# Performance work log

Measured on AMD Instinct MI355X. Metric: run time of the kernel, lower is better.

The kernel has to match this reference:

```python
import jax, jax.numpy as jnp
import numpy as np

D = 256                      # covariance dim, hardcoded by bottleneck Conv2d(_, 256, 1)
ITER_N = 5                   # SqrtmLayer(output, 5)
_r, _c = np.triu_indices(D)
FLAT_IDX = jnp.asarray(_r * D + _c)   # upper-tri (incl. diag) indices into flattened d*d


def setup_inputs() -> dict:
    key = jax.random.key(0)
    ks = jax.random.split(key, 5)
    B, C, H, W = 64, 2048, 16, 16
    num_classes = 4
    feats = D * (D + 1) // 2  # 32896
    return {
        "features": jax.random.normal(ks[0], (B, C, H, W), jnp.float32),
        "w_bn": jax.random.normal(ks[1], (D, C), jnp.float32) * 0.02,
        "b_bn": jnp.zeros((D,), jnp.float32),
        "w_type": jax.random.normal(ks[2], (num_classes, feats), jnp.float32) * 0.01,
        "b_type": jnp.zeros((num_classes,), jnp.float32),
        "w_flag": jax.random.normal(ks[3], (1, feats), jnp.float32) * 0.01,
        "b_flag": jnp.zeros((1,), jnp.float32),
    }


def _covpool(x):
    # x: [B, d, h, w] -> second-order pooling: x_f @ I_hat @ x_f^T, equivalent
    # to (1/M) * centered @ centered^T  (I_hat = -1/M^2 * ones + 1/M * eye)
    B, d, h, w = x.shape
    M = h * w
    xf = x.reshape(B, d, M)
    centered = xf - xf.mean(axis=2, keepdims=True)
    return jnp.einsum('bim,bjm->bij', centered, centered) / M  # [B, d, d]


def _sqrtm_ns(A, iter_n=ITER_N):
    # Newton-Schulz iteration for matrix square root (iSQRT-COV style)
    B, d, _ = A.shape
    I3 = 3.0 * jnp.eye(d, dtype=A.dtype)
    normA = jnp.trace(A, axis1=1, axis2=2)          # [B], pre-normalization
    An = A / normA[:, None, None]
    ZY = 0.5 * (I3 - An)
    Y = jnp.matmul(An, ZY)
    Z = ZY
    for _ in range(iter_n - 2):
        ZY = 0.5 * (I3 - jnp.matmul(Z, Y))
        Y = jnp.matmul(Y, ZY)
        Z = jnp.matmul(ZY, Z)
    YZY = 0.5 * jnp.matmul(Y, I3 - jnp.matmul(Z, Y))
    return YZY * jnp.sqrt(normA)[:, None, None]     # post-compensation


def reference(features, w_bn, b_bn, w_type, b_type, w_flag, b_flag):
    # 1x1 bottleneck conv: [B, C, H, W] -> [B, 256, H, W]
    x = jnp.einsum('bchw,oc->bohw', features, w_bn) + b_bn[None, :, None, None]
    cov = _covpool(x)                # [B, 256, 256]
    s = _sqrtm_ns(cov)               # [B, 256, 256]
    B = s.shape[0]
    vec = s.reshape(B, D * D)[:, FLAT_IDX]   # triu-vec: [B, 32896]
    type_logits = vec @ w_type.T + b_type    # [B, num_classes]
    flag_logits = vec @ w_flag.T + b_flag    # [B, 1]
    return (type_logits, flag_logits)
```

## Files before the change

kernel.cpp:

```cpp
#include <hip/hip_runtime.h>
#include <math.h>


typedef __attribute__((ext_vector_type(8))) short bf16x8;
typedef __attribute__((ext_vector_type(4))) float f32x4;
typedef __attribute__((ext_vector_type(4))) unsigned u32x4;
typedef __attribute__((ext_vector_type(2))) unsigned u32x2;

__device__ __forceinline__ unsigned fbits(float f) { union { float f; unsigned u; } x; x.f = f; return x.u; }
__device__ __forceinline__ float bitsf(unsigned u) { union { float f; unsigned u; } x; x.u = u; return x.f; }
__device__ __forceinline__ float bf16v(short h) { return bitsf(((unsigned)(unsigned short)h) << 16); }

__device__ __forceinline__ unsigned pack_h(float a, float b) {
  return (fbits(a) >> 16) | (fbits(b) & 0xFFFF0000u);
}
__device__ __forceinline__ unsigned pack_l(float a, float b) {
  float la = a - bitsf(fbits(a) & 0xFFFF0000u);
  float lb = b - bitsf(fbits(b) & 0xFFFF0000u);
  return (fbits(la) >> 16) | (fbits(lb) & 0xFFFF0000u);
}

__device__ __forceinline__ const bf16x8* fragp(const char* M, int kt, int row,
                                               int g, int pl) {
  return (const bf16x8*)(M + (size_t)kt * 32768 + (size_t)row * 128 +
                         ((((pl << 2) + g) ^ (row & 7)) << 4));
}
__device__ __forceinline__ const bf16x8* fragl(const char* L, int kt, int row,
                                               int g, int pl) {
  return (const bf16x8*)(L + kt * 8192 + row * 128 +
                         ((((pl << 2) + g) ^ (row & 7)) << 4));
}

__device__ __forceinline__ void write_quad_g(char* M, int row, int k0,
                                             const float* v) {
  char* rp = M + (size_t)(k0 >> 5) * 32768 + (size_t)row * 128;
  const int s = (k0 & 31) >> 3, bo = (k0 & 7) * 2;
  *(u32x2*)(rp + (((s) ^ (row & 7)) << 4) + bo) =
      (u32x2){pack_h(v[0], v[1]), pack_h(v[2], v[3])};
  *(u32x2*)(rp + (((s + 4) ^ (row & 7)) << 4) + bo) =
      (u32x2){pack_l(v[0], v[1]), pack_l(v[2], v[3])};
}
__device__ __forceinline__ void write_quad_l(char* L, int row, int k0,
                                             const float* v) {
  char* rp = L + (k0 >> 5) * 8192 + row * 128;
  const int s = (k0 & 31) >> 3, bo = (k0 & 7) * 2;
  *(u32x2*)(rp + (((s) ^ (row & 7)) << 4) + bo) =
      (u32x2){pack_h(v[0], v[1]), pack_h(v[2], v[3])};
  *(u32x2*)(rp + (((s + 4) ^ (row & 7)) << 4) + bo) =
      (u32x2){pack_l(v[0], v[1]), pack_l(v[2], v[3])};
}
__device__ __forceinline__ void read_quad_g(const char* M, int row, int k0,
                                            float* v) {
  const char* rp = M + (size_t)(k0 >> 5) * 32768 + (size_t)row * 128;
  const int s = (k0 & 31) >> 3, bo = (k0 & 7) * 2;
  const u32x2 hq = *(const u32x2*)(rp + (((s) ^ (row & 7)) << 4) + bo);
  const u32x2 lq = *(const u32x2*)(rp + (((s + 4) ^ (row & 7)) << 4) + bo);
  v[0] = bitsf(hq[0] << 16) + bitsf(lq[0] << 16);
  v[1] = bitsf(hq[0] & 0xFFFF0000u) + bitsf(lq[0] & 0xFFFF0000u);
  v[2] = bitsf(hq[1] << 16) + bitsf(lq[1] << 16);
  v[3] = bitsf(hq[1] & 0xFFFF0000u) + bitsf(lq[1] & 0xFFFF0000u);
}

#define MFMA3(c, aH, aL, bH, bL)                                            \
  c = __builtin_amdgcn_mfma_f32_16x16x32_bf16(aL, bH, c, 0, 0, 0);          \
  c = __builtin_amdgcn_mfma_f32_16x16x32_bf16(aH, bL, c, 0, 0, 0);          \
  c = __builtin_amdgcn_mfma_f32_16x16x32_bf16(aH, bH, c, 0, 0, 0);

#define LGKM_BAR() do { asm volatile("s_waitcnt lgkmcnt(0)" ::: "memory"); \
                        __builtin_amdgcn_s_barrier(); } while (0)

__global__ __launch_bounds__(256) void prep_k(
    const float* __restrict__ w_bn, const float* __restrict__ w_type,
    const float* __restrict__ w_flag, char* __restrict__ Wf,
    float* __restrict__ W2)
{
  const int bid = blockIdx.x;
  if (bid < 64) {
    const int kt = bid, r = threadIdx.x;
    const float* src = w_bn + (size_t)r * 2048 + kt * 32;
    char* rp = Wf + (size_t)kt * 32768 + (size_t)r * 128;
#pragma unroll
    for (int s = 0; s < 4; ++s) {
      float x[8];
#pragma unroll
      for (int e = 0; e < 8; ++e) x[e] = src[s * 8 + e];
      *(u32x4*)(rp + ((s ^ (r & 7)) << 4)) =
          (u32x4){pack_h(x[0], x[1]), pack_h(x[2], x[3]),
                  pack_h(x[4], x[5]), pack_h(x[6], x[7])};
      *(u32x4*)(rp + (((s + 4) ^ (r & 7)) << 4)) =
          (u32x4){pack_l(x[0], x[1]), pack_l(x[2], x[3]),
                  pack_l(x[4], x[5]), pack_l(x[6], x[7])};
    }
  } else {
    const int idx = bid - 64;
    const int v = idx >> 6, chunk = idx & 63;
    const float* src = (v < 4) ? (w_type + (size_t)v * 32896) : w_flag;
    const int e0 = chunk * 1024 + threadIdx.x * 4;
#pragma unroll
    for (int q = 0; q < 4; ++q) {
      const int e = e0 + q;
      const int i = e >> 8, j = e & 255;
      const int r = i < j ? i : j, c = i < j ? j : i;
      const int t = r * 256 - (r * (r - 1)) / 2 + (c - r);
      W2[(size_t)v * 65536 + e] = src[t] * (i == j ? 1.0f : 0.5f);
    }
  }
}

__global__ __launch_bounds__(512) void conv5_k(
    const char* __restrict__ Wf, const float* __restrict__ F,
    float* __restrict__ Xpart)
{
  __shared__ float bf32[2][64 * 33];
  __shared__ __align__(16) char bfmt[2][8192];

  const int tid = threadIdx.x, lane = tid & 63, w = tid >> 6;
  const int wr = w >> 1, wc = w & 1, fr = lane & 15, g = lane >> 4;
  const int jb = blockIdx.x * 64, bz = blockIdx.y, ks = blockIdx.z;
  const int kb = ks * 32;
  const float* Fb = F + (size_t)bz * 524288;

  const int blc = tid >> 4, blpx = (tid & 15) * 4;
  const int pkpx = tid >> 3, pkq = tid & 3, pkpl = (tid >> 2) & 1;

  f32x4 acc[4][2] = {};
  bf16x8 pa0[4][2], pa1[4][2];
  float4 bl0, bl1;

  auto bload = [&](int t, float4& r) {
    r = *(const float4*)(Fb + ((size_t)(kb + t) * 32 + blc) * 256 + jb + blpx);
  };
  auto bf32w = [&](int buf, const float4& r) {
    float* p = &bf32[buf][0];
    p[(blpx + 0) * 33 + blc] = r.x;
    p[(blpx + 1) * 33 + blc] = r.y;
    p[(blpx + 2) * 33 + blc] = r.z;
    p[(blpx + 3) * 33 + blc] = r.w;
  };
  auto aload = [&](int t, bf16x8 (*pa)[2]) {
#pragma unroll
    for (int m = 0; m < 4; ++m) {
      const int r = wr * 64 + m * 16 + fr;
#pragma unroll
      for (int pl = 0; pl < 2; ++pl) pa[m][pl] = *fragp(Wf, kb + t, r, g, pl);
    }
  };
  auto pack = [&](int buf) {
    const float* p = &bf32[buf][pkpx * 33 + pkq * 8];
    float x[8];
#pragma unroll
    for (int e = 0; e < 8; ++e) x[e] = p[e];
    u32x4 outv;
    if (pkpl == 0)
      outv = (u32x4){pack_h(x[0], x[1]), pack_h(x[2], x[3]),
                     pack_h(x[4], x[5]), pack_h(x[6], x[7])};
    else
      outv = (u32x4){pack_l(x[0], x[1]), pack_l(x[2], x[3]),
                     pack_l(x[4], x[5]), pack_l(x[6], x[7])};
    const int slot = ((pkpl << 2) + pkq) ^ (pkpx & 7);
    *(u32x4*)(&bfmt[buf][pkpx * 128 + slot * 16]) = outv;
  };
  auto gemmstep = [&](int buf, bf16x8 (*pa)[2]) {
    bf16x8 bH[2], bL[2];
#pragma unroll
    for (int n = 0; n < 2; ++n) {
      const int r = wc * 32 + n * 16 + fr;
      const char* rp = &bfmt[buf][r * 128];
      bH[n] = *(const bf16x8*)(rp + ((g ^ (r & 7)) << 4));
      bL[n] = *(const bf16x8*)(rp + (((g + 4) ^ (r & 7)) << 4));
    }
#pragma unroll
    for (int m = 0; m < 4; ++m)
#pragma unroll
      for (int n = 0; n < 2; ++n) {
        f32x4 c = acc[m][n];
        MFMA3(c, pa[m][0], pa[m][1], bH[n], bL[n]);
        acc[m][n] = c;
      }
  };

  bload(0, bl0);
  bf32w(0, bl0);
  bload(1, bl1);
  aload(0, pa0);
  LGKM_BAR();
  bf32w(1, bl1);
  pack(0);
  aload(1, pa1);
  bload(2, bl0);
  LGKM_BAR();

  for (int t2 = 0; t2 < 32; t2 += 2) {
    gemmstep(0, pa0);
    if (t2 + 1 < 32) pack(1);
    if (t2 + 2 < 32) { bf32w(0, bl0); aload(t2 + 2, pa0); }
    if (t2 + 3 < 32) bload(t2 + 3, bl1);
    LGKM_BAR();
    gemmstep(1, pa1);
    if (t2 + 2 < 32) pack(0);
    if (t2 + 3 < 32) { bf32w(1, bl1); aload(t2 + 3, pa1); }
    if (t2 + 4 < 32) bload(t2 + 4, bl0);
    LGKM_BAR();
  }

  float* Xp = Xpart + ((size_t)ks * 64 + bz) * 65536;
#pragma unroll
  for (int m = 0; m < 4; ++m) {
    const int gi0 = wr * 64 + m * 16 + g * 4;
#pragma unroll
    for (int n = 0; n < 2; ++n) {
      const int gj = jb + wc * 32 + n * 16 + fr;
#pragma unroll
      for (int j = 0; j < 4; ++j)
        Xp[(size_t)(gi0 + j) * 256 + gj] = acc[m][n][j];
    }
  }
}

__global__ __launch_bounds__(256) void combine_k(
    const float* __restrict__ Xp0, const float* __restrict__ Xp1,
    const float* __restrict__ bias, char* __restrict__ X,
    float* __restrict__ mu, float* __restrict__ nrm_part)
{
  const int chunk = blockIdx.x, bz = blockIdx.y;
  const int tid = threadIdx.x, lane = tid & 63, w = tid >> 6;
  const float* p0 = Xp0 + (size_t)bz * 65536;
  const float* p1 = Xp1 + (size_t)bz * 65536;
  char* Xb = X + (size_t)bz * 262144;
  float tracc = 0.f;
#pragma unroll
  for (int i = 0; i < 8; ++i) {
    const int r = chunk * 32 + w * 8 + i;
    const float4 a = *(const float4*)(p0 + (size_t)r * 256 + lane * 4);
    const float4 b = *(const float4*)(p1 + (size_t)r * 256 + lane * 4);
    const float bi = bias[r];
    float v[4] = {a.x + b.x + bi, a.y + b.y + bi,
                  a.z + b.z + bi, a.w + b.w + bi};
    float s = v[0] + v[1] + v[2] + v[3];
    float ss = v[0] * v[0] + v[1] * v[1] + v[2] * v[2] + v[3] * v[3];
#pragma unroll
    for (int o = 32; o > 0; o >>= 1) {
      s += __shfl_down(s, o);
      ss += __shfl_down(ss, o);
    }
    const float st = __shfl(s, 0), sst = __shfl(ss, 0);
    const float m = st * (1.f / 256.f);
    if (lane == 0) mu[bz * 256 + r] = m;
    tracc += sst * (1.f / 256.f) - m * m;
    write_quad_g(Xb, r, lane * 4, v);
  }
  __shared__ float red[4];
  if (lane == 0) red[w] = tracc;
  __syncthreads();
  if (tid == 0)
    nrm_part[bz * 8 + chunk] = red[0] + red[1] + red[2] + red[3];
}

__device__ __forceinline__ float nrm_sum(const float* nrmp, int bz) {
  float nv = 0.f;
#pragma unroll
  for (int q = 0; q < 8; ++q) nv += nrmp[bz * 8 + q];
  return nv;
}

template <int MODE>
__global__ __launch_bounds__(512) void col_k(
    const char* __restrict__ A1, const char* __restrict__ Bsrc,
    const char* __restrict__ Ys, const char* __restrict__ Zs,
    char* __restrict__ outA, char* __restrict__ outB,
    const float* __restrict__ mu, const float* __restrict__ nrmp,
    float* __restrict__ Sf)
{
  __shared__ __align__(16) char Plds[65536];
  const int tid = threadIdx.x, lane = tid & 63, w = tid >> 6;
  const int fr = lane & 15, g = lane >> 4;
  const int blk = blockIdx.x;
  const int bz = (blk & 7) * 8 + ((blk >> 3) & 7);
  const int jb = (blk >> 6) * 64;
  const size_t MB = 262144;
  const char* Ab = A1 + (size_t)bz * MB;
  const char* Bb = Bsrc + (size_t)bz * MB;
  const int r0 = g * 4;

  f32x4 acc[2][4] = {};
  {
    bf16x8 pa[2][2][2], pb[2][4][2];
#pragma unroll
    for (int par = 0; par < 2; ++par) {
#pragma unroll
      for (int m = 0; m < 2; ++m) {
        const int r = w * 32 + m * 16 + fr;
#pragma unroll
        for (int pl = 0; pl < 2; ++pl) pa[par][m][pl] = *fragp(Ab, par, r, g, pl);
      }
#pragma unroll
      for (int n = 0; n < 4; ++n) {
        const int r = jb + n * 16 + fr;
#pragma unroll
        for (int pl = 0; pl < 2; ++pl) pb[par][n][pl] = *fragp(Bb, par, r, g, pl);
      }
    }
    for (int t2 = 0; t2 < 8; t2 += 2) {
#pragma unroll
      for (int par = 0; par < 2; ++par) {
        const int t = t2 + par;
        bf16x8 aH[2], aL[2], bH[4], bL[4];
#pragma unroll
        for (int m = 0; m < 2; ++m) { aH[m] = pa[par][m][0]; aL[m] = pa[par][m][1]; }
#pragma unroll
        for (int n = 0; n < 4; ++n) { bH[n] = pb[par][n][0]; bL[n] = pb[par][n][1]; }
        if (t + 2 < 8) {
#pragma unroll
          for (int m = 0; m < 2; ++m) {
            const int r = w * 32 + m * 16 + fr;
#pragma unroll
            for (int pl = 0; pl < 2; ++pl)
              pa[par][m][pl] = *fragp(Ab, t + 2, r, g, pl);
          }
#pragma unroll
          for (int n = 0; n < 4; ++n) {
            const int r = jb + n * 16 + fr;
#pragma unroll
            for (int pl = 0; pl < 2; ++pl)
              pb[par][n][pl] = *fragp(Bb, t + 2, r, g, pl);
          }
        }
#pragma unroll
        for (int m = 0; m < 2; ++m)
#pragma unroll
          for (int n = 0; n < 4; ++n) {
            f32x4 c = acc[m][n];
            MFMA3(c, aH[m], aL[m], bH[n], bL[n]);
            acc[m][n] = c;
          }
      }
    }
  }

  if constexpr (MODE == 0) {
    const float rn = 1.0f / nrm_sum(nrmp, bz);
    const float* mub = mu + bz * 256;
    char* oA = outA + (size_t)bz * MB;
    char* oB = outB + (size_t)bz * MB;
#pragma unroll
    for (int m = 0; m < 2; ++m) {
      const int gi0 = w * 32 + m * 16 + r0;
#pragma unroll
      for (int n = 0; n < 4; ++n) {
        const int gj = jb + n * 16 + fr;
        float vv[4], zz[4];
#pragma unroll
        for (int j = 0; j < 4; ++j) {
          const float v =
              (acc[m][n][j] * (1.f / 256.f) - mub[gi0 + j] * mub[gj]) * rn;
          vv[j] = v;
          zz[j] = (gi0 + j == gj ? 1.5f : 0.f) - 0.5f * v;
        }
        write_quad_g(oA, gj, gi0, vv);
        write_quad_g(oB, gj, gi0, zz);
      }
    }
  } else if constexpr (MODE == 1) {
    char* oA = outA + (size_t)bz * MB;
#pragma unroll
    for (int m = 0; m < 2; ++m) {
      const int gi0 = w * 32 + m * 16 + r0;
#pragma unroll
      for (int n = 0; n < 4; ++n) {
        const int gj = jb + n * 16 + fr;
        float av[4], vv[4];
        read_quad_g(Bb, gj, gi0, av);
#pragma unroll
        for (int j = 0; j < 4; ++j) vv[j] = 1.5f * av[j] - 0.5f * acc[m][n][j];
        write_quad_g(oA, gj, gi0, vv);
      }
    }
  } else {
#pragma unroll
    for (int m = 0; m < 2; ++m) {
      const int gi0 = w * 32 + m * 16 + r0;
#pragma unroll
      for (int n = 0; n < 4; ++n) {
        const int jl = n * 16 + fr;
        float vv[4] = {acc[m][n][0], acc[m][n][1], acc[m][n][2], acc[m][n][3]};
        write_quad_l(Plds, jl, gi0, vv);
      }
    }
    const char* Yb = Ys + (size_t)bz * MB;
    const char* Zb = (MODE == 2) ? (Zs + (size_t)bz * MB) : nullptr;
    bf16x8 py[2][2][2], pz[2][2][2];
#pragma unroll
    for (int par = 0; par < 2; ++par)
#pragma unroll
      for (int m = 0; m < 2; ++m) {
        const int r = w * 32 + m * 16 + fr;
#pragma unroll
        for (int pl = 0; pl < 2; ++pl) {
          py[par][m][pl] = *fragp(Yb, par, r, g, pl);
          if constexpr (MODE == 2) pz[par][m][pl] = *fragp(Zb, par, r, g, pl);
        }
      }
    __syncthreads();

    f32x4 aY[2][4] = {}, aZ[2][4] = {};
    for (int t2 = 0; t2 < 8; t2 += 2) {
#pragma unroll
      for (int par = 0; par < 2; ++par) {
        const int t = t2 + par;
        bf16x8 yH[2], yL[2], zH[2], zL[2];
#pragma unroll
        for (int m = 0; m < 2; ++m) {
          yH[m] = py[par][m][0]; yL[m] = py[par][m][1];
          if constexpr (MODE == 2) { zH[m] = pz[par][m][0]; zL[m] = pz[par][m][1]; }
        }
        if (t + 2 < 8) {
#pragma unroll
          for (int m = 0; m < 2; ++m) {
            const int r = w * 32 + m * 16 + fr;
#pragma unroll
            for (int pl = 0; pl < 2; ++pl) {
              py[par][m][pl] = *fragp(Yb, t + 2, r, g, pl);
              if constexpr (MODE == 2) pz[par][m][pl] = *fragp(Zb, t + 2, r, g, pl);
            }
          }
        }
        bf16x8 bH[4], bL[4];
#pragma unroll
        for (int n = 0; n < 4; ++n) {
          const int jl = n * 16 + fr;
          bH[n] = *fragl(Plds, t, jl, g, 0);
          bL[n] = *fragl(Plds, t, jl, g, 1);
        }
#pragma unroll
        for (int m = 0; m < 2; ++m)
#pragma unroll
          for (int n = 0; n < 4; ++n) {
            f32x4 cy = aY[m][n];
            MFMA3(cy, yH[m], yL[m], bH[n], bL[n]);
            aY[m][n] = cy;
            if constexpr (MODE == 2) {
              f32x4 cz = aZ[m][n];
              MFMA3(cz, zH[m], zL[m], bH[n], bL[n]);
              aZ[m][n] = cz;
            }
          }
      }
    }
    if constexpr (MODE == 2) {
      char* oA = outA + (size_t)bz * MB;
      char* oB = outB + (size_t)bz * MB;
#pragma unroll
      for (int m = 0; m < 2; ++m) {
        const int gi0 = w * 32 + m * 16 + r0;
#pragma unroll
        for (int n = 0; n < 4; ++n) {
          const int gj = jb + n * 16 + fr;
          float base[4], vv[4];
          read_quad_g(Yb, gj, gi0, base);
#pragma unroll
          for (int j = 0; j < 4; ++j) vv[j] = 1.5f * base[j] - 0.5f * aY[m][n][j];
          write_quad_g(oA, gj, gi0, vv);
          read_quad_g(Zb, gj, gi0, base);
#pragma unroll
          for (int j = 0; j < 4; ++j) vv[j] = 1.5f * base[j] - 0.5f * aZ[m][n][j];
          write_quad_g(oB, gj, gi0, vv);
        }
      }
    } else {
      const float sq = sqrtf(nrm_sum(nrmp, bz));
      float* Sb = Sf + (size_t)bz * 65536;
#pragma unroll
      for (int m = 0; m < 2; ++m) {
        const int gi0 = w * 32 + m * 16 + r0;
#pragma unroll
        for (int n = 0; n < 4; ++n) {
          const int gj = jb + n * 16 + fr;
          float base[4];
          read_quad_g(Yb, gj, gi0, base);
          f32x4 vv;
#pragma unroll
          for (int j = 0; j < 4; ++j)
            vv[j] = (1.5f * base[j] - 0.5f * aY[m][n][j]) * sq;
          *(f32x4*)(Sb + (size_t)gj * 256 + gi0) = vv;
        }
      }
    }
  }
}

__global__ __launch_bounds__(256) void head2(
    const float* __restrict__ Sf, const float* __restrict__ W2,
    const float* __restrict__ b_type, const float* __restrict__ b_flag,
    float* __restrict__ out)
{
  const int b = blockIdx.x, v = blockIdx.y, tid = threadIdx.x;
  const float4* s4 = (const float4*)(Sf + (size_t)b * 65536);
  const float4* w4 = (const float4*)(W2 + (size_t)v * 65536);
  float acc = 0.f;
  for (int i = tid; i < 16384; i += 256) {
    const float4 a = s4[i], c = w4[i];
    acc += a.x * c.x + a.y * c.y + a.z * c.z + a.w * c.w;
  }
  __shared__ float red[256];
  red[tid] = acc;
  __syncthreads();
  for (int o = 128; o > 0; o >>= 1) {
    if (tid < o) red[tid] += red[tid + o];
    __syncthreads();
  }
  if (tid == 0) {
    if (v < 4) out[b * 4 + v] = red[0] + b_type[v];
    else       out[256 + b] = red[0] + b_flag[0];
  }
}

extern "C" void kernel_launch(void* const* d_in, const int* in_sizes, int n_in,
                              void* d_out, int out_size, void* d_ws, size_t ws_size,
                              hipStream_t stream)
{
  const float* features = (const float*)d_in[0];
  const float* w_bn     = (const float*)d_in[1];
  const float* b_bn     = (const float*)d_in[2];
  const float* w_type   = (const float*)d_in[3];
  const float* b_type   = (const float*)d_in[4];
  const float* w_flag   = (const float*)d_in[5];
  const float* b_flag   = (const float*)d_in[6];
  float* out = (float*)d_out;

  char* W = (char*)d_ws;
  const size_t PB = 16777216;
  char* P0 = W;           char* P1 = W + PB;     char* P2 = W + 2 * PB;
  char* P3 = W + 3 * PB;  char* P4 = W + 4 * PB;
  char* Wf = W + 5 * PB;
  float* W2 = (float*)(W + 5 * PB + 2097152);
  float* mu = (float*)(W + 5 * PB + 4194304);
  float* nrm_part = mu + 16384;
  float* Xpart = (float*)(W + 5 * PB + 8388608);
  float* Sf = (float*)P4;

  prep_k<<<dim3(384), dim3(256), 0, stream>>>(w_bn, w_type, w_flag, Wf, W2);
  conv5_k<<<dim3(4, 64, 2), dim3(512), 0, stream>>>(Wf, features, Xpart);
  combine_k<<<dim3(8, 64), dim3(256), 0, stream>>>(
      Xpart, Xpart + 64ull * 65536, b_bn, P0, mu, nrm_part);

  const dim3 cg(256), cb(512);
  col_k<0><<<cg, cb, 0, stream>>>(P0, P0, nullptr, nullptr, P1, P2, mu, nrm_part, nullptr);
  col_k<1><<<cg, cb, 0, stream>>>(P1, P1, nullptr, nullptr, P3, nullptr, nullptr, nullptr, nullptr);
  col_k<2><<<cg, cb, 0, stream>>>(P2, P3, P3, P2, P0, P4, nullptr, nullptr, nullptr);
  col_k<2><<<cg, cb, 0, stream>>>(P4, P0, P0, P4, P1, P2, nullptr, nullptr, nullptr);
  col_k<2><<<cg, cb, 0, stream>>>(P2, P1, P1, P2, P3, P0, nullptr, nullptr, nullptr);
  col_k<3><<<cg, cb, 0, stream>>>(P0, P3, P3, nullptr, nullptr, nullptr, nullptr, nrm_part, Sf);

  head2<<<dim3(64, 5), dim3(256), 0, stream>>>(Sf, W2, b_type, b_flag, out);
  (void)in_sizes; (void)n_in; (void)out_size; (void)ws_size;
}
```

Measured before the change: 287.1 us.

## Deepen conv GEMM pipeline to two k-tiles per stage with more global prefetch

```diff
diff --git a/kernel.cpp b/kernel.cpp
--- a/kernel.cpp
+++ b/kernel.cpp
@@ -107,12 +107,12 @@
   }
 }
 
-__global__ __launch_bounds__(512) void conv5_k(
+__global__ __launch_bounds__(512) void conv6_k(
     const char* __restrict__ Wf, const float* __restrict__ F,
     float* __restrict__ Xpart)
 {
-  __shared__ float bf32[2][64 * 33];
-  __shared__ __align__(16) char bfmt[2][8192];
+  __shared__ float bf32s[2][64 * 33];
+  __shared__ __align__(16) char bfmt[2][2][8192];
 
   const int tid = threadIdx.x, lane = tid & 63, w = tid >> 6;
   const int wr = w >> 1, wc = w & 1, fr = lane & 15, g = lane >> 4;
@@ -124,14 +124,13 @@
   const int pkpx = tid >> 3, pkq = tid & 3, pkpl = (tid >> 2) & 1;
 
   f32x4 acc[4][2] = {};
-  bf16x8 pa0[4][2], pa1[4][2];
-  float4 bl0, bl1;
-
-  auto bload = [&](int t, float4& r) {
-    r = *(const float4*)(Fb + ((size_t)(kb + t) * 32 + blc) * 256 + jb + blpx);
+  bf16x8 paA[4][2], paB[4][2];
+
+  auto bload = [&](int t) -> float4 {
+    return *(const float4*)(Fb + ((size_t)(kb + t) * 32 + blc) * 256 + jb + blpx);
   };
-  auto bf32w = [&](int buf, const float4& r) {
-    float* p = &bf32[buf][0];
+  auto bf32w = [&](int kk, const float4& r) {
+    float* p = &bf32s[kk][0];
     p[(blpx + 0) * 33 + blc] = r.x;
     p[(blpx + 1) * 33 + blc] = r.y;
     p[(blpx + 2) * 33 + blc] = r.z;
@@ -145,8 +144,8 @@
       for (int pl = 0; pl < 2; ++pl) pa[m][pl] = *fragp(Wf, kb + t, r, g, pl);
     }
   };
-  auto pack = [&](int buf) {
-    const float* p = &bf32[buf][pkpx * 33 + pkq * 8];
+  auto pack = [&](int kk, int dq) {
+    const float* p = &bf32s[kk][pkpx * 33 + pkq * 8];
     float x[8];
 #pragma unroll
     for (int e = 0; e < 8; ++e) x[e] = p[e];
@@ -158,14 +157,14 @@
       outv = (u32x4){pack_l(x[0], x[1]), pack_l(x[2], x[3]),
                      pack_l(x[4], x[5]), pack_l(x[6], x[7])};
     const int slot = ((pkpl << 2) + pkq) ^ (pkpx & 7);
-    *(u32x4*)(&bfmt[buf][pkpx * 128 + slot * 16]) = outv;
+    *(u32x4*)(&bfmt[dq][kk][pkpx * 128 + slot * 16]) = outv;
   };
-  auto gemmstep = [&](int buf, bf16x8 (*pa)[2]) {
+  auto gemmstep = [&](int sq, int kk, bf16x8 (*pa)[2]) {
     bf16x8 bH[2], bL[2];
 #pragma unroll
     for (int n = 0; n < 2; ++n) {
       const int r = wc * 32 + n * 16 + fr;
-      const char* rp = &bfmt[buf][r * 128];
+      const char* rp = &bfmt[sq][kk][r * 128];
       bH[n] = *(const bf16x8*)(rp + ((g ^ (r & 7)) << 4));
       bL[n] = *(const bf16x8*)(rp + (((g + 4) ^ (r & 7)) << 4));
     }
@@ -179,27 +178,37 @@
       }
   };
 
-  bload(0, bl0);
-  bf32w(0, bl0);
-  bload(1, bl1);
-  aload(0, pa0);
+  float4 b0 = bload(0), b1 = bload(1), b2 = bload(2), b3 = bload(3);
+  float4 blE0 = bload(4), blE1 = bload(5);
+  float4 blO0 = bload(6), blO1 = bload(7);
+  aload(0, paA);
+  aload(1, paB);
+
+  bf32w(0, b0); bf32w(1, b1);
   LGKM_BAR();
-  bf32w(1, bl1);
-  pack(0);
-  aload(1, pa1);
-  bload(2, bl0);
+  pack(0, 0); pack(1, 0);
   LGKM_BAR();
-
-  for (int t2 = 0; t2 < 32; t2 += 2) {
-    gemmstep(0, pa0);
-    if (t2 + 1 < 32) pack(1);
-    if (t2 + 2 < 32) { bf32w(0, bl0); aload(t2 + 2, pa0); }
-    if (t2 + 3 < 32) bload(t2 + 3, bl1);
+  bf32w(0, b2); bf32w(1, b3);
+  LGKM_BAR();
+
+  for (int pp = 0; pp < 8; ++pp) {
+    const int k4 = 4 * pp;
+    gemmstep(0, 0, paA);
+    gemmstep(0, 1, paB);
+    aload(k4 + 2, paA);
+    aload(k4 + 3, paB);
+    pack(0, 1); pack(1, 1);
     LGKM_BAR();
-    gemmstep(1, pa1);
-    if (t2 + 2 < 32) pack(0);
-    if (t2 + 3 < 32) { bf32w(1, bl1); aload(t2 + 3, pa1); }
-    if (t2 + 4 < 32) bload(t2 + 4, bl0);
+    if (pp < 7) { bf32w(0, blE0); bf32w(1, blE1); }
+    if (pp < 6) { blE0 = bload(k4 + 8); blE1 = bload(k4 + 9); }
+    LGKM_BAR();
+    gemmstep(1, 0, paA);
+    gemmstep(1, 1, paB);
+    if (pp < 7) { aload(k4 + 4, paA); aload(k4 + 5, paB); }
+    if (pp < 7) { pack(0, 0); pack(1, 0); }
+    LGKM_BAR();
+    if (pp < 7) { bf32w(0, blO0); bf32w(1, blO1); }
+    if (pp < 6) { blO0 = bload(k4 + 10); blO1 = bload(k4 + 11); }
     LGKM_BAR();
   }
 
@@ -539,7 +548,7 @@
   float* Sf = (float*)P4;
 
   prep_k<<<dim3(384), dim3(256), 0, stream>>>(w_bn, w_type, w_flag, Wf, W2);
-  conv5_k<<<dim3(4, 64, 2), dim3(512), 0, stream>>>(Wf, features, Xpart);
+  conv6_k<<<dim3(4, 64, 2), dim3(512), 0, stream>>>(Wf, features, Xpart);
   combine_k<<<dim3(8, 64), dim3(256), 0, stream>>>(
       Xpart, Xpart + 64ull * 65536, b_bn, P0, mu, nrm_part);
 
```

After: 274.4 us. -4.4%, faster.

## Load conv B-fragments directly from global and store S in head-friendly order

Applied to the files above, without the earlier changes.

```diff
diff --git a/kernel.cpp b/kernel.cpp
--- a/kernel.cpp
+++ b/kernel.cpp
@@ -9,7 +9,6 @@
 
 __device__ __forceinline__ unsigned fbits(float f) { union { float f; unsigned u; } x; x.f = f; return x.u; }
 __device__ __forceinline__ float bitsf(unsigned u) { union { float f; unsigned u; } x; x.u = u; return x.f; }
-__device__ __forceinline__ float bf16v(short h) { return bitsf(((unsigned)(unsigned short)h) << 16); }
 
 __device__ __forceinline__ unsigned pack_h(float a, float b) {
   return (fbits(a) >> 16) | (fbits(b) & 0xFFFF0000u);
@@ -66,9 +65,6 @@
   c = __builtin_amdgcn_mfma_f32_16x16x32_bf16(aH, bL, c, 0, 0, 0);          \
   c = __builtin_amdgcn_mfma_f32_16x16x32_bf16(aH, bH, c, 0, 0, 0);
 
-#define LGKM_BAR() do { asm volatile("s_waitcnt lgkmcnt(0)" ::: "memory"); \
-                        __builtin_amdgcn_s_barrier(); } while (0)
-
 __global__ __launch_bounds__(256) void prep_k(
     const float* __restrict__ w_bn, const float* __restrict__ w_type,
     const float* __restrict__ w_flag, char* __restrict__ Wf,
@@ -93,82 +89,74 @@
     }
   } else {
     const int idx = bid - 64;
-    const int v = idx >> 6, chunk = idx & 63;
+    const int v = idx >> 4, chunk = idx & 15;
     const float* src = (v < 4) ? (w_type + (size_t)v * 32896) : w_flag;
-    const int e0 = chunk * 1024 + threadIdx.x * 4;
-#pragma unroll
-    for (int q = 0; q < 4; ++q) {
-      const int e = e0 + q;
-      const int i = e >> 8, j = e & 255;
-      const int r = i < j ? i : j, c = i < j ? j : i;
-      const int t = r * 256 - (r * (r - 1)) / 2 + (c - r);
-      W2[(size_t)v * 65536 + e] = src[t] * (i == j ? 1.0f : 0.5f);
-    }
-  }
-}
-
-__global__ __launch_bounds__(512) void conv5_k(
+    const int s0 = chunk * 4096 + threadIdx.x * 16;
+    float outv[16];
+#pragma unroll
+    for (int q = 0; q < 16; ++q) {
+      const int s = s0 + q;
+      const int jbp = s >> 14, r = s & 16383;
+      const int ttid = r >> 5, qq = r & 31;
+      const int m = qq >> 4, n = (qq >> 2) & 3, jj = qq & 3;
+      const int ww = ttid >> 6, ll = ttid & 63;
+      const int i = ww * 32 + m * 16 + (ll >> 4) * 4 + jj;
+      const int jcol = jbp * 64 + n * 16 + (ll & 15);
+      const int rr = i < jcol ? i : jcol, cc = i < jcol ? jcol : i;
+      const int t = rr * 256 - (rr * (rr - 1)) / 2 + (cc - rr);
+      outv[q] = src[t] * (i == jcol ? 1.0f : 0.5f);
+    }
+    float* dst = W2 + (size_t)v * 65536 + s0;
+#pragma unroll
+    for (int q = 0; q < 4; ++q)
+      *(f32x4*)(dst + q * 4) = *(f32x4*)(outv + q * 4);
+  }
+}
+
+__global__ __launch_bounds__(512) void conv7_k(
     const char* __restrict__ Wf, const float* __restrict__ F,
     float* __restrict__ Xpart)
 {
-  __shared__ float bf32[2][64 * 33];
-  __shared__ __align__(16) char bfmt[2][8192];
-
   const int tid = threadIdx.x, lane = tid & 63, w = tid >> 6;
   const int wr = w >> 1, wc = w & 1, fr = lane & 15, g = lane >> 4;
   const int jb = blockIdx.x * 64, bz = blockIdx.y, ks = blockIdx.z;
   const int kb = ks * 32;
-  const float* Fb = F + (size_t)bz * 524288;
-
-  const int blc = tid >> 4, blpx = (tid & 15) * 4;
-  const int pkpx = tid >> 3, pkq = tid & 3, pkpl = (tid >> 2) & 1;
+  const float* Fb = F + (size_t)bz * 524288 + jb + wc * 32 + fr;
 
   f32x4 acc[4][2] = {};
-  bf16x8 pa0[4][2], pa1[4][2];
-  float4 bl0, bl1;
-
-  auto bload = [&](int t, float4& r) {
-    r = *(const float4*)(Fb + ((size_t)(kb + t) * 32 + blc) * 256 + jb + blpx);
+  bf16x8 pa[4][2];
+  float bA[16], bB[16];
+
+  auto bload = [&](int t, float* d) {
+    const float* s = Fb + ((size_t)(kb + t) * 32 + g * 8) * 256;
+#pragma unroll
+    for (int n = 0; n < 2; ++n)
+#pragma unroll
+      for (int e = 0; e < 8; ++e) d[n * 8 + e] = s[(size_t)e * 256 + n * 16];
   };
-  auto bf32w = [&](int buf, const float4& r) {
-    float* p = &bf32[buf][0];
-    p[(blpx + 0) * 33 + blc] = r.x;
-    p[(blpx + 1) * 33 + blc] = r.y;
-    p[(blpx + 2) * 33 + blc] = r.z;
-    p[(blpx + 3) * 33 + blc] = r.w;
+  auto aload = [&](int t) {
+#pragma unroll
+    for (int m = 0; m < 4; ++m)
+#pragma unroll
+      for (int pl = 0; pl < 2; ++pl)
+        pa[m][pl] = *fragp(Wf, kb + t, wr * 64 + m * 16 + fr, g, pl);
   };
-  auto aload = [&](int t, bf16x8 (*pa)[2]) {
-#pragma unroll
-    for (int m = 0; m < 4; ++m) {
-      const int r = wr * 64 + m * 16 + fr;
-#pragma unroll
-      for (int pl = 0; pl < 2; ++pl) pa[m][pl] = *fragp(Wf, kb + t, r, g, pl);
+  auto packfrag = [&](const float* x, bf16x8* bH, bf16x8* bL) {
+#pragma unroll
+    for (int n = 0; n < 2; ++n) {
+      short hh[8], ll[8];
+#pragma unroll
+      for (int e = 0; e < 8; ++e) {
+        const float v = x[n * 8 + e];
+        const unsigned u = fbits(v);
+        hh[e] = (short)(u >> 16);
+        ll[e] = (short)(fbits(v - bitsf(u & 0xFFFF0000u)) >> 16);
+      }
+      bH[n] = *(bf16x8*)hh;
+      bL[n] = *(bf16x8*)ll;
     }
   };
-  auto pack = [&](int buf) {
-    const float* p = &bf32[buf][pkpx * 33 + pkq * 8];
-    float x[8];
-#pragma unroll
-    for (int e = 0; e < 8; ++e) x[e] = p[e];
-    u32x4 outv;
-    if (pkpl == 0)
-      outv = (u32x4){pack_h(x[0], x[1]), pack_h(x[2], x[3]),
-                     pack_h(x[4], x[5]), pack_h(x[6], x[7])};
-    else
-      outv = (u32x4){pack_l(x[0], x[1]), pack_l(x[2], x[3]),
-                     pack_l(x[4], x[5]), pack_l(x[6], x[7])};
-    const int slot = ((pkpl << 2) + pkq) ^ (pkpx & 7);
-    *(u32x4*)(&bfmt[buf][pkpx * 128 + slot * 16]) = outv;
-  };
-  auto gemmstep = [&](int buf, bf16x8 (*pa)[2]) {
-    bf16x8 bH[2], bL[2];
-#pragma unroll
-    for (int n = 0; n < 2; ++n) {
-      const int r = wc * 32 + n * 16 + fr;
-      const char* rp = &bfmt[buf][r * 128];
-      bH[n] = *(const bf16x8*)(rp + ((g ^ (r & 7)) << 4));
-      bL[n] = *(const bf16x8*)(rp + (((g + 4) ^ (r & 7)) << 4));
-    }
+  auto gemm24 = [&](const bf16x8* bH, const bf16x8* bL) {
 #pragma unroll
     for (int m = 0; m < 4; ++m)
 #pragma unroll
@@ -179,28 +167,19 @@
       }
   };
 
-  bload(0, bl0);
-  bf32w(0, bl0);
-  bload(1, bl1);
-  aload(0, pa0);
-  LGKM_BAR();
-  bf32w(1, bl1);
-  pack(0);
-  aload(1, pa1);
-  bload(2, bl0);
-  LGKM_BAR();
-
+  bload(0, bA);
+  bload(1, bB);
+  aload(0);
   for (int t2 = 0; t2 < 32; t2 += 2) {
-    gemmstep(0, pa0);
-    if (t2 + 1 < 32) pack(1);
-    if (t2 + 2 < 32) { bf32w(0, bl0); aload(t2 + 2, pa0); }
-    if (t2 + 3 < 32) bload(t2 + 3, bl1);
-    LGKM_BAR();
-    gemmstep(1, pa1);
-    if (t2 + 2 < 32) pack(0);
-    if (t2 + 3 < 32) { bf32w(1, bl1); aload(t2 + 3, pa1); }
-    if (t2 + 4 < 32) bload(t2 + 4, bl0);
-    LGKM_BAR();
+    bf16x8 bH[2], bL[2];
+    packfrag(bA, bH, bL);
+    gemm24(bH, bL);
+    aload(t2 + 1);
+    if (t2 + 2 < 32) bload(t2 + 2, bA);
+    packfrag(bB, bH, bL);
+    gemm24(bH, bL);
+    if (t2 + 2 < 32) aload(t2 + 2);
+    if (t2 + 3 < 32) bload(t2 + 3, bB);
   }
 
   float* Xp = Xpart + ((size_t)ks * 64 + bz) * 65536;
@@ -276,7 +255,8 @@
   const int fr = lane & 15, g = lane >> 4;
   const int blk = blockIdx.x;
   const int bz = (blk & 7) * 8 + ((blk >> 3) & 7);
-  const int jb = (blk >> 6) * 64;
+  const int jbp = blk >> 6;
+  const int jb = jbp * 64;
   const size_t MB = 262144;
   const char* Ab = A1 + (size_t)bz * MB;
   const char* Bb = Bsrc + (size_t)bz * MB;
@@ -468,7 +448,7 @@
       }
     } else {
       const float sq = sqrtf(nrm_sum(nrmp, bz));
-      float* Sb = Sf + (size_t)bz * 65536;
+      float* Sb = Sf + (size_t)bz * 65536 + (size_t)jbp * 16384 + (size_t)tid * 32;
 #pragma unroll
       for (int m = 0; m < 2; ++m) {
         const int gi0 = w * 32 + m * 16 + r0;
@@ -481,7 +461,7 @@
 #pragma unroll
           for (int j = 0; j < 4; ++j)
             vv[j] = (1.5f * base[j] - 0.5f * aY[m][n][j]) * sq;
-          *(f32x4*)(Sb + (size_t)gj * 256 + gi0) = vv;
+          *(f32x4*)(Sb + m * 16 + n * 4) = vv;
         }
       }
     }
@@ -538,8 +518,8 @@
   float* Xpart = (float*)(W + 5 * PB + 8388608);
   float* Sf = (float*)P4;
 
-  prep_k<<<dim3(384), dim3(256), 0, stream>>>(w_bn, w_type, w_flag, Wf, W2);
-  conv5_k<<<dim3(4, 64, 2), dim3(512), 0, stream>>>(Wf, features, Xpart);
+  prep_k<<<dim3(144), dim3(256), 0, stream>>>(w_bn, w_type, w_flag, Wf, W2);
+  conv7_k<<<dim3(4, 64, 2), dim3(512), 0, stream>>>(Wf, features, Xpart);
   combine_k<<<dim3(8, 64), dim3(256), 0, stream>>>(
       Xpart, Xpart + 64ull * 65536, b_bn, P0, mu, nrm_part);
 
```

Result: no change. 292.6 us (+1.9%).
